# Kernel optimization log

Measured on AMD Instinct MI355X. Metric: run time of the kernel, lower is better.

Reference implementation:

```python
import jax, jax.numpy as jnp
import numpy as np

H, W, C = 64, 64, 128
HEADS, DIM_HEAD = 4, 32
DIM = HEADS * DIM_HEAD
SCALE = 10.0
EPS = 1e-08


def setup_inputs() -> dict:
    key = jax.random.key(0)
    k1, k2, k3, k4 = jax.random.split(key, 4)
    x = jax.random.normal(k1, (H, W, C), dtype=jnp.float32)
    # 1x1 conv kernels act as plain channel-mixing matrices
    w_in = jax.random.normal(k2, (3 * DIM, C), dtype=jnp.float32) * (1.0 / np.sqrt(C))
    w_out = jax.random.normal(k3, (C, DIM), dtype=jnp.float32) * (1.0 / np.sqrt(DIM))
    b_out = jax.random.normal(k4, (C,), dtype=jnp.float32) * 0.01
    return {"x": x, "w_in": w_in, "w_out": w_out, "b_out": b_out}


def reference(x, w_in, w_out, b_out):
    HW = H * W
    # conv_in: 1x1 conv == channel matmul -> (HW, 3, heads, dim_head)
    qkv = jnp.einsum('hwc,oc->hwo', x, w_in).reshape(HW, 3, HEADS, DIM_HEAD)
    q, k, v = qkv[:, 0], qkv[:, 1], qkv[:, 2]  # each (HW, h, d)

    def normalize(t):
        # L2 norm over the sequence axis (axis=0), as in the source
        n = jnp.sqrt(jnp.sum(t * t, axis=0, keepdims=True))
        return t / jnp.clip(n, EPS)

    q = normalize(q)
    k = normalize(k)
    sim = jnp.einsum('ihd,jhd->hij', q, k) * SCALE  # (h, HW, HW)
    attn = jax.nn.softmax(sim, axis=-1)
    out = jnp.einsum('hij,jhd->hid', attn, v)  # (h, HW, d)
    # 'h (H W) d -> H W (h d)'
    out = out.transpose(1, 0, 2).reshape(H, W, DIM)
    # conv_out: 1x1 conv with bias
    out = jnp.einsum('hwd,cd->hwc', out, w_out) + b_out
    return out
```

## Files before the change

kernel.cpp:

```cpp
#include <hip/hip_runtime.h>
#include <hip/hip_bf16.h>


typedef float  f32x4 __attribute__((ext_vector_type(4)));
typedef short  s16x8 __attribute__((ext_vector_type(8)));
typedef unsigned short u16x4 __attribute__((ext_vector_type(4)));
typedef unsigned short u16;

__device__ __forceinline__ u16 f2bf(float f) {
  unsigned int u = __float_as_uint(f);
  u += 0x7FFFu + ((u >> 16) & 1u);
  return (u16)(u >> 16);
}
__device__ __forceinline__ float bf2f(u16 u) {
  return __uint_as_float(((unsigned int)u) << 16);
}
__device__ __forceinline__ s16x8 load8f_bf16(const float* p) {
  const f32x4* q = (const f32x4*)p;
  f32x4 a = q[0], b = q[1];
  s16x8 r;
  r[0]=(short)f2bf(a[0]); r[1]=(short)f2bf(a[1]); r[2]=(short)f2bf(a[2]); r[3]=(short)f2bf(a[3]);
  r[4]=(short)f2bf(b[0]); r[5]=(short)f2bf(b[1]); r[6]=(short)f2bf(b[2]); r[7]=(short)f2bf(b[3]);
  return r;
}

__global__ __launch_bounds__(256) void qkv_kernel(
    const float* __restrict__ x, const float* __restrict__ w_in,
    u16* __restrict__ Qb, u16* __restrict__ Kb, u16* __restrict__ Vtb,
    float* __restrict__ part_sq) {
  __shared__ float sqpart[2][128];
  const int tid = threadIdx.x;
  const int w = tid >> 6, lane = tid & 63, li = lane & 15, kg = lane >> 4;
  const int wm = w & 1, wn = w >> 1;
  const int g = blockIdx.y;
  const int mb = blockIdx.x;
  const int irow = mb * 32 + wm * 16;

  s16x8 ax[4];
#pragma unroll
  for (int kc = 0; kc < 4; ++kc)
    ax[kc] = load8f_bf16(x + (size_t)(irow + li) * 128 + kc * 32 + kg * 8);

  const float* W = w_in + (size_t)g * 128 * 128;
#pragma unroll
  for (int nt = 0; nt < 4; ++nt) {
    const int colrel = wn * 64 + nt * 16 + li;
    f32x4 acc = {0.f, 0.f, 0.f, 0.f};
#pragma unroll
    for (int kc = 0; kc < 4; ++kc) {
      s16x8 bw = load8f_bf16(W + (size_t)colrel * 128 + kc * 32 + kg * 8);
      acc = __builtin_amdgcn_mfma_f32_16x16x32_bf16(ax[kc], bw, acc, 0, 0, 0);
    }
    const int h = colrel >> 5, d = colrel & 31;
    const int r0 = irow + kg * 4;
    if (g == 2) {
      u16x4 pv;
#pragma unroll
      for (int r = 0; r < 4; ++r) pv[r] = f2bf(acc[r]);
      *(u16x4*)(Vtb + ((size_t)(h * 32 + d) * 4096 + r0)) = pv;
    } else {
      float ss = acc[0]*acc[0] + acc[1]*acc[1] + acc[2]*acc[2] + acc[3]*acc[3];
      ss += __shfl_xor(ss, 16);
      ss += __shfl_xor(ss, 32);
      if (lane < 16) sqpart[wm][colrel] = ss;
      u16* dst = (g == 0 ? Qb : Kb);
#pragma unroll
      for (int r = 0; r < 4; ++r)
        dst[((size_t)h * 4096 + r0 + r) * 32 + d] = f2bf(acc[r]);
    }
  }
  __syncthreads();
  if (g < 2 && tid < 128)
    part_sq[((size_t)g * 128 + tid) * 128 + mb] = sqpart[0][tid] + sqpart[1][tid];
}

__global__ __launch_bounds__(1024, 4) void attn_kernel(
    const u16* __restrict__ Qb, const u16* __restrict__ Kb,
    const u16* __restrict__ Vtb, const float* __restrict__ part_sq,
    float* __restrict__ Oat, float* __restrict__ denom) {
  __shared__ __align__(16) char lds[99456];
  const int tid = threadIdx.x;
  const int w = tid >> 6, lane = tid & 63, li = lane & 15, kg = lane >> 4;
  const int wq = w >> 2, wk = w & 3;
  const int h = blockIdx.y, q0 = blockIdx.x * 64;
  float* dl  = (float*)(lds + 98304);
  float* scs = (float*)(lds + 99328);
  const u16* Kh = Kb  + (size_t)h * 4096 * 32;
  const u16* Vh = Vtb + (size_t)h * 32 * 4096;
  const int jl = tid >> 2, sl = tid & 3;
  const int dv = tid >> 5, sv = tid & 31;

  {
    s16x8 kreg = *(const s16x8*)(Kh + (size_t)jl * 32 + sl * 8);
    s16x8 vreg = *(const s16x8*)(Vh + (size_t)dv * 4096 + sv * 8);
    *(s16x8*)(lds + jl * 64 + ((sl * 16) ^ ((jl & 7) << 4))) = kreg;
    *(s16x8*)(lds + 32768 + dv * 512 + ((sv * 16) ^ ((dv & 7) << 4))) = vreg;
  }
  if (w == 0) {
    const int kind = lane >> 5, d = lane & 31;
    const f32x4* p4 = (const f32x4*)(part_sq + (size_t)(kind * 128 + h * 32 + d) * 128);
    float sum = 0.f;
#pragma unroll
    for (int m = 0; m < 32; ++m) { f32x4 v = p4[m]; sum += (v[0]+v[1]) + (v[2]+v[3]); }
    float n = fmaxf(sqrtf(sum), 1e-8f);
    float other = __shfl_xor(n, 32);
    if (lane < 32) scs[lane] = 10.f / (n * other);
  }
  __syncthreads();

  s16x8 aq;
  {
    const u16* qp = Qb + ((size_t)h * 4096 + q0 + wq * 16 + li) * 32 + kg * 8;
    s16x8 qr = *(const s16x8*)qp;
#pragma unroll
    for (int e = 0; e < 8; ++e) aq[e] = (short)f2bf(bf2f((u16)qr[e]) * scs[kg * 8 + e]);
  }

  f32x4 acc0 = {0,0,0,0}, acc1 = {0,0,0,0};
  float sden = 0.f;
  const int psw  = (li & 7) << 4;
  char* Pslab = lds + 65536 + w * 2048 + li * 128;
  const int kswz = (kg * 16) ^ psw;

  int cur = 0;
  for (int jt = 0; jt < 16; ++jt) {
    s16x8 kreg = {}, vreg = {};
    if (jt < 15) {
      const int j0n = (jt + 1) * 256;
      kreg = *(const s16x8*)(Kh + (size_t)(j0n + jl) * 32 + sl * 8);
      vreg = *(const s16x8*)(Vh + (size_t)dv * 4096 + j0n + sv * 8);
    }
    const char* Kc = lds + cur * 16384;
    const char* Vc = lds + 32768 + cur * 16384;
    f32x4 st[4];
#pragma unroll
    for (int jb = 0; jb < 4; ++jb) {
      s16x8 kf = *(const s16x8*)(Kc + (wk * 64 + jb * 16 + li) * 64 + kswz);
      f32x4 z = {0, 0, 0, 0};
      st[jb] = __builtin_amdgcn_mfma_f32_16x16x32_bf16(kf, aq, z, 0, 0, 0);
    }
#pragma unroll
    for (int jb = 0; jb < 4; ++jb) {
      float p0 = __expf(st[jb][0]), p1 = __expf(st[jb][1]);
      float p2 = __expf(st[jb][2]), p3 = __expf(st[jb][3]);
      sden += (p0 + p1) + (p2 + p3);
      uint2 pk;
      pk.x = (unsigned)f2bf(p0) | ((unsigned)f2bf(p1) << 16);
      pk.y = (unsigned)f2bf(p2) | ((unsigned)f2bf(p3) << 16);
      *(uint2*)(Pslab + ((jb * 32 + kg * 8) ^ psw)) = pk;
    }
#pragma unroll
    for (int c = 0; c < 2; ++c) {
      s16x8 ap = *(const s16x8*)(Pslab + ((c * 64 + kg * 16) ^ psw));
      const int vsw = ((wk * 8 + c * 4 + kg) * 16) ^ psw;
      s16x8 vf0 = *(const s16x8*)(Vc + li * 512 + vsw);
      s16x8 vf1 = *(const s16x8*)(Vc + (li + 16) * 512 + vsw);
      acc0 = __builtin_amdgcn_mfma_f32_16x16x32_bf16(ap, vf0, acc0, 0, 0, 0);
      acc1 = __builtin_amdgcn_mfma_f32_16x16x32_bf16(ap, vf1, acc1, 0, 0, 0);
    }
    __syncthreads();
    if (jt < 15) {
      char* Kn = lds + (cur ^ 1) * 16384;
      char* Vn = lds + 32768 + (cur ^ 1) * 16384;
      *(s16x8*)(Kn + jl * 64 + ((sl * 16) ^ ((jl & 7) << 4))) = kreg;
      *(s16x8*)(Vn + dv * 512 + ((sv * 16) ^ ((dv & 7) << 4))) = vreg;
    }
    __syncthreads();
    cur ^= 1;
  }

  sden += __shfl_xor(sden, 16);
  sden += __shfl_xor(sden, 32);
  if (lane < 16) dl[w * 16 + li] = sden;
  float* comb = (float*)lds;
#pragma unroll
  for (int r = 0; r < 4; ++r) {
    comb[(w * 16 + kg * 4 + r) * 32 + li]      = acc0[r];
    comb[(w * 16 + kg * 4 + r) * 32 + 16 + li] = acc1[r];
  }
  __syncthreads();
  {
    const int row = tid >> 4, cp = (tid & 15) * 2;
    const int wb = (row >> 4) * 4, r16 = row & 15;
    float o0 = 0.f, o1 = 0.f;
#pragma unroll
    for (int k2 = 0; k2 < 4; ++k2) {
      const float* src = comb + ((wb + k2) * 16 + r16) * 32 + cp;
      o0 += src[0]; o1 += src[1];
    }
    float2 o2 = {o0, o1};
    *(float2*)(Oat + (size_t)(q0 + row) * 128 + h * 32 + cp) = o2;
    if (tid < 64) {
      float ds = 0.f;
#pragma unroll
      for (int k2 = 0; k2 < 4; ++k2) ds += dl[((tid >> 4) * 4 + k2) * 16 + (tid & 15)];
      denom[(size_t)h * 4096 + q0 + tid] = ds;
    }
  }
}

__global__ __launch_bounds__(256) void proj_kernel(
    const float* __restrict__ Oat, const float* __restrict__ denom,
    const float* __restrict__ w_out, const float* __restrict__ b_out,
    float* __restrict__ out) {
  const int tid = threadIdx.x;
  const int w = tid >> 6, lane = tid & 63, li = lane & 15, kg = lane >> 4;
  const int i0 = blockIdx.x * 16;
  const int n0 = blockIdx.y * 64;
  const int i = i0 + li;

  s16x8 ao[4];
#pragma unroll
  for (int kc = 0; kc < 4; ++kc) {
    const float inv = 1.f / denom[(size_t)kc * 4096 + i];
    const f32x4* p = (const f32x4*)(Oat + (size_t)i * 128 + kc * 32 + kg * 8);
    f32x4 a = p[0], b = p[1];
    s16x8 r;
    r[0]=(short)f2bf(a[0]*inv); r[1]=(short)f2bf(a[1]*inv);
    r[2]=(short)f2bf(a[2]*inv); r[3]=(short)f2bf(a[3]*inv);
    r[4]=(short)f2bf(b[0]*inv); r[5]=(short)f2bf(b[1]*inv);
    r[6]=(short)f2bf(b[2]*inv); r[7]=(short)f2bf(b[3]*inv);
    ao[kc] = r;
  }
  const int c = n0 + w * 16 + li;
  f32x4 acc = {0, 0, 0, 0};
#pragma unroll
  for (int kc = 0; kc < 4; ++kc) {
    s16x8 bw = load8f_bf16(w_out + (size_t)c * 128 + kc * 32 + kg * 8);
    acc = __builtin_amdgcn_mfma_f32_16x16x32_bf16(ao[kc], bw, acc, 0, 0, 0);
  }
  const float bias = b_out[c];
#pragma unroll
  for (int r = 0; r < 4; ++r)
    out[(size_t)(i0 + kg * 4 + r) * 128 + c] = acc[r] + bias;
}

extern "C" void kernel_launch(void* const* d_in, const int* in_sizes, int n_in,
                              void* d_out, int out_size, void* d_ws, size_t ws_size,
                              hipStream_t stream) {
  const float* x     = (const float*)d_in[0];
  const float* w_in  = (const float*)d_in[1];
  const float* w_out = (const float*)d_in[2];
  const float* b_out = (const float*)d_in[3];
  float* out = (float*)d_out;

  char* ws = (char*)d_ws;
  float* Oat     = (float*)ws;
  float* denom   = (float*)(ws + 2097152);
  float* part_sq = (float*)(ws + 2097152 + 65536);
  u16*   Qb  = (u16*)(ws + 2097152 + 65536 + 131072);
  u16*   Kb  = (u16*)(ws + 2097152 + 65536 + 131072 + 1048576);
  u16*   Vtb = (u16*)(ws + 2097152 + 65536 + 131072 + 2 * 1048576);

  qkv_kernel <<<dim3(128, 3), 256,  0, stream>>>(x, w_in, Qb, Kb, Vtb, part_sq);
  attn_kernel<<<dim3(64, 4),  1024, 0, stream>>>(Qb, Kb, Vtb, part_sq, Oat, denom);
  proj_kernel<<<dim3(256, 2), 256,  0, stream>>>(Oat, denom, w_out, b_out, out);
}
```

Before: 102.2 us.

## Fuse QKV, attention and projection into one cooperative kernel with grid syncs

```diff
diff --git a/kernel.cpp b/kernel.cpp
--- a/kernel.cpp
+++ b/kernel.cpp
@@ -1,5 +1,7 @@
 #include <hip/hip_runtime.h>
 #include <hip/hip_bf16.h>
+#include <hip/hip_cooperative_groups.h>
+namespace cg = cooperative_groups;
 
 
 typedef float  f32x4 __attribute__((ext_vector_type(4)));
@@ -24,215 +26,199 @@
   return r;
 }
 
-__global__ __launch_bounds__(256) void qkv_kernel(
+__global__ __launch_bounds__(1024, 4) void fused_kernel(
     const float* __restrict__ x, const float* __restrict__ w_in,
+    const float* __restrict__ w_out, const float* __restrict__ b_out,
     u16* __restrict__ Qb, u16* __restrict__ Kb, u16* __restrict__ Vtb,
-    float* __restrict__ part_sq) {
-  __shared__ float sqpart[2][128];
-  const int tid = threadIdx.x;
-  const int w = tid >> 6, lane = tid & 63, li = lane & 15, kg = lane >> 4;
-  const int wm = w & 1, wn = w >> 1;
-  const int g = blockIdx.y;
-  const int mb = blockIdx.x;
-  const int irow = mb * 32 + wm * 16;
-
-  s16x8 ax[4];
-#pragma unroll
-  for (int kc = 0; kc < 4; ++kc)
-    ax[kc] = load8f_bf16(x + (size_t)(irow + li) * 128 + kc * 32 + kg * 8);
-
-  const float* W = w_in + (size_t)g * 128 * 128;
-#pragma unroll
-  for (int nt = 0; nt < 4; ++nt) {
-    const int colrel = wn * 64 + nt * 16 + li;
-    f32x4 acc = {0.f, 0.f, 0.f, 0.f};
-#pragma unroll
-    for (int kc = 0; kc < 4; ++kc) {
-      s16x8 bw = load8f_bf16(W + (size_t)colrel * 128 + kc * 32 + kg * 8);
-      acc = __builtin_amdgcn_mfma_f32_16x16x32_bf16(ax[kc], bw, acc, 0, 0, 0);
-    }
-    const int h = colrel >> 5, d = colrel & 31;
-    const int r0 = irow + kg * 4;
-    if (g == 2) {
-      u16x4 pv;
-#pragma unroll
-      for (int r = 0; r < 4; ++r) pv[r] = f2bf(acc[r]);
-      *(u16x4*)(Vtb + ((size_t)(h * 32 + d) * 4096 + r0)) = pv;
-    } else {
-      float ss = acc[0]*acc[0] + acc[1]*acc[1] + acc[2]*acc[2] + acc[3]*acc[3];
-      ss += __shfl_xor(ss, 16);
-      ss += __shfl_xor(ss, 32);
-      if (lane < 16) sqpart[wm][colrel] = ss;
-      u16* dst = (g == 0 ? Qb : Kb);
-#pragma unroll
-      for (int r = 0; r < 4; ++r)
-        dst[((size_t)h * 4096 + r0 + r) * 32 + d] = f2bf(acc[r]);
-    }
-  }
-  __syncthreads();
-  if (g < 2 && tid < 128)
-    part_sq[((size_t)g * 128 + tid) * 128 + mb] = sqpart[0][tid] + sqpart[1][tid];
-}
-
-__global__ __launch_bounds__(1024, 4) void attn_kernel(
-    const u16* __restrict__ Qb, const u16* __restrict__ Kb,
-    const u16* __restrict__ Vtb, const float* __restrict__ part_sq,
-    float* __restrict__ Oat, float* __restrict__ denom) {
+    float* __restrict__ sq, float* __restrict__ Oat,
+    float* __restrict__ denom, float* __restrict__ out) {
   __shared__ __align__(16) char lds[99456];
   const int tid = threadIdx.x;
   const int w = tid >> 6, lane = tid & 63, li = lane & 15, kg = lane >> 4;
-  const int wq = w >> 2, wk = w & 3;
-  const int h = blockIdx.y, q0 = blockIdx.x * 64;
-  float* dl  = (float*)(lds + 98304);
-  float* scs = (float*)(lds + 99328);
-  const u16* Kh = Kb  + (size_t)h * 4096 * 32;
-  const u16* Vh = Vtb + (size_t)h * 32 * 4096;
-  const int jl = tid >> 2, sl = tid & 3;
-  const int dv = tid >> 5, sv = tid & 31;
+  const int b = blockIdx.x;
 
   {
-    s16x8 kreg = *(const s16x8*)(Kh + (size_t)jl * 32 + sl * 8);
-    s16x8 vreg = *(const s16x8*)(Vh + (size_t)dv * 4096 + sv * 8);
-    *(s16x8*)(lds + jl * 64 + ((sl * 16) ^ ((jl & 7) << 4))) = kreg;
-    *(s16x8*)(lds + 32768 + dv * 512 + ((sv * 16) ^ ((dv & 7) << 4))) = vreg;
+    const int r0 = b * 16;
+    s16x8 ax[4];
+#pragma unroll
+    for (int kc = 0; kc < 4; ++kc)
+      ax[kc] = load8f_bf16(x + (size_t)(r0 + li) * 128 + kc * 32 + kg * 8);
+    for (int t = w; t < 24; t += 16) {
+      const int c = t * 16 + li;
+      f32x4 acc = {0.f, 0.f, 0.f, 0.f};
+#pragma unroll
+      for (int kc = 0; kc < 4; ++kc) {
+        s16x8 bw = load8f_bf16(w_in + (size_t)c * 128 + kc * 32 + kg * 8);
+        acc = __builtin_amdgcn_mfma_f32_16x16x32_bf16(ax[kc], bw, acc, 0, 0, 0);
+      }
+      const int g = c >> 7, colrel = c & 127;
+      const int h2 = colrel >> 5, d = colrel & 31;
+      const int rr = r0 + kg * 4;
+      if (g == 2) {
+        u16x4 pv;
+#pragma unroll
+        for (int r = 0; r < 4; ++r) pv[r] = f2bf(acc[r]);
+        *(u16x4*)(Vtb + ((size_t)(h2 * 32 + d) * 4096 + rr)) = pv;
+      } else {
+        float ss = acc[0]*acc[0] + acc[1]*acc[1] + acc[2]*acc[2] + acc[3]*acc[3];
+        ss += __shfl_xor(ss, 16);
+        ss += __shfl_xor(ss, 32);
+        u16* dst = (g == 0 ? Qb : Kb);
+#pragma unroll
+        for (int r = 0; r < 4; ++r)
+          dst[((size_t)h2 * 4096 + rr + r) * 32 + d] = f2bf(acc[r]);
+        if (lane < 16) atomicAdd(sq + g * 128 + colrel, ss);
+      }
+    }
   }
-  if (w == 0) {
-    const int kind = lane >> 5, d = lane & 31;
-    const f32x4* p4 = (const f32x4*)(part_sq + (size_t)(kind * 128 + h * 32 + d) * 128);
-    float sum = 0.f;
-#pragma unroll
-    for (int m = 0; m < 32; ++m) { f32x4 v = p4[m]; sum += (v[0]+v[1]) + (v[2]+v[3]); }
-    float n = fmaxf(sqrtf(sum), 1e-8f);
-    float other = __shfl_xor(n, 32);
-    if (lane < 32) scs[lane] = 10.f / (n * other);
+  __threadfence();
+  cg::this_grid().sync();
+
+  {
+    const int h = b >> 6, q0 = (b & 63) * 64;
+    const int wq = w >> 2, wk = w & 3;
+    float* dl  = (float*)(lds + 98304);
+    float* scs = (float*)(lds + 99328);
+    const u16* Kh = Kb  + (size_t)h * 4096 * 32;
+    const u16* Vh = Vtb + (size_t)h * 32 * 4096;
+    const int jl = tid >> 2, sl = tid & 3;
+    const int dv = tid >> 5, sv = tid & 31;
+
+    {
+      s16x8 kreg = *(const s16x8*)(Kh + (size_t)jl * 32 + sl * 8);
+      s16x8 vreg = *(const s16x8*)(Vh + (size_t)dv * 4096 + sv * 8);
+      *(s16x8*)(lds + jl * 64 + ((sl * 16) ^ ((jl & 7) << 4))) = kreg;
+      *(s16x8*)(lds + 32768 + dv * 512 + ((sv * 16) ^ ((dv & 7) << 4))) = vreg;
+    }
+    if (w == 0) {
+      const int kind = lane >> 5, d = lane & 31;
+      float n = fmaxf(sqrtf(sq[kind * 128 + h * 32 + d]), 1e-8f);
+      float other = __shfl_xor(n, 32);
+      if (lane < 32) scs[lane] = 10.f / (n * other);
+    }
+    __syncthreads();
+
+    s16x8 aq;
+    {
+      const u16* qp = Qb + ((size_t)h * 4096 + q0 + wq * 16 + li) * 32 + kg * 8;
+      s16x8 qr = *(const s16x8*)qp;
+#pragma unroll
+      for (int e = 0; e < 8; ++e) aq[e] = (short)f2bf(bf2f((u16)qr[e]) * scs[kg * 8 + e]);
+    }
+
+    f32x4 acc0 = {0,0,0,0}, acc1 = {0,0,0,0};
+    float sden = 0.f;
+    const int psw  = (li & 7) << 4;
+    char* Pslab = lds + 65536 + w * 2048 + li * 128;
+    const int kswz = (kg * 16) ^ psw;
+
+    int cur = 0;
+    for (int jt = 0; jt < 16; ++jt) {
+      s16x8 kreg = {}, vreg = {};
+      if (jt < 15) {
+        const int j0n = (jt + 1) * 256;
+        kreg = *(const s16x8*)(Kh + (size_t)(j0n + jl) * 32 + sl * 8);
+        vreg = *(const s16x8*)(Vh + (size_t)dv * 4096 + j0n + sv * 8);
+      }
+      const char* Kc = lds + cur * 16384;
+      const char* Vc = lds + 32768 + cur * 16384;
+      f32x4 st[4];
+#pragma unroll
+      for (int jb = 0; jb < 4; ++jb) {
+        s16x8 kf = *(const s16x8*)(Kc + (wk * 64 + jb * 16 + li) * 64 + kswz);
+        f32x4 z = {0, 0, 0, 0};
+        st[jb] = __builtin_amdgcn_mfma_f32_16x16x32_bf16(kf, aq, z, 0, 0, 0);
+      }
+#pragma unroll
+      for (int jb = 0; jb < 4; ++jb) {
+        float p0 = __expf(st[jb][0]), p1 = __expf(st[jb][1]);
+        float p2 = __expf(st[jb][2]), p3 = __expf(st[jb][3]);
+        sden += (p0 + p1) + (p2 + p3);
+        uint2 pk;
+        pk.x = (unsigned)f2bf(p0) | ((unsigned)f2bf(p1) << 16);
+        pk.y = (unsigned)f2bf(p2) | ((unsigned)f2bf(p3) << 16);
+        *(uint2*)(Pslab + ((jb * 32 + kg * 8) ^ psw)) = pk;
+      }
+#pragma unroll
+      for (int c = 0; c < 2; ++c) {
+        s16x8 ap = *(const s16x8*)(Pslab + ((c * 64 + kg * 16) ^ psw));
+        const int vsw = ((wk * 8 + c * 4 + kg) * 16) ^ psw;
+        s16x8 vf0 = *(const s16x8*)(Vc + li * 512 + vsw);
+        s16x8 vf1 = *(const s16x8*)(Vc + (li + 16) * 512 + vsw);
+        acc0 = __builtin_amdgcn_mfma_f32_16x16x32_bf16(ap, vf0, acc0, 0, 0, 0);
+        acc1 = __builtin_amdgcn_mfma_f32_16x16x32_bf16(ap, vf1, acc1, 0, 0, 0);
+      }
+      __syncthreads();
+      if (jt < 15) {
+        char* Kn = lds + (cur ^ 1) * 16384;
+        char* Vn = lds + 32768 + (cur ^ 1) * 16384;
+        *(s16x8*)(Kn + jl * 64 + ((sl * 16) ^ ((jl & 7) << 4))) = kreg;
+        *(s16x8*)(Vn + dv * 512 + ((sv * 16) ^ ((dv & 7) << 4))) = vreg;
+      }
+      __syncthreads();
+      cur ^= 1;
+    }
+
+    sden += __shfl_xor(sden, 16);
+    sden += __shfl_xor(sden, 32);
+    if (lane < 16) dl[w * 16 + li] = sden;
+    float* comb = (float*)lds;
+#pragma unroll
+    for (int r = 0; r < 4; ++r) {
+      comb[(w * 16 + kg * 4 + r) * 32 + li]      = acc0[r];
+      comb[(w * 16 + kg * 4 + r) * 32 + 16 + li] = acc1[r];
+    }
+    __syncthreads();
+    {
+      const int row = tid >> 4, cp = (tid & 15) * 2;
+      const int wb = (row >> 4) * 4, r16 = row & 15;
+      float o0 = 0.f, o1 = 0.f;
+#pragma unroll
+      for (int k2 = 0; k2 < 4; ++k2) {
+        const float* src = comb + ((wb + k2) * 16 + r16) * 32 + cp;
+        o0 += src[0]; o1 += src[1];
+      }
+      float2 o2 = {o0, o1};
+      *(float2*)(Oat + (size_t)(q0 + row) * 128 + h * 32 + cp) = o2;
+      if (tid < 64) {
+        float ds = 0.f;
+#pragma unroll
+        for (int k2 = 0; k2 < 4; ++k2) ds += dl[((tid >> 4) * 4 + k2) * 16 + (tid & 15)];
+        denom[(size_t)h * 4096 + q0 + tid] = ds;
+      }
+    }
   }
-  __syncthreads();
-
-  s16x8 aq;
-  {
-    const u16* qp = Qb + ((size_t)h * 4096 + q0 + wq * 16 + li) * 32 + kg * 8;
-    s16x8 qr = *(const s16x8*)qp;
-#pragma unroll
-    for (int e = 0; e < 8; ++e) aq[e] = (short)f2bf(bf2f((u16)qr[e]) * scs[kg * 8 + e]);
+  __threadfence();
+  cg::this_grid().sync();
+
+  if (w < 8) {
+    const int i0 = b * 16;
+    const int i = i0 + li;
+    s16x8 ao[4];
+#pragma unroll
+    for (int kc = 0; kc < 4; ++kc) {
+      const float inv = 1.f / denom[(size_t)kc * 4096 + i];
+      const f32x4* p = (const f32x4*)(Oat + (size_t)i * 128 + kc * 32 + kg * 8);
+      f32x4 a = p[0], bb = p[1];
+      s16x8 r;
+      r[0]=(short)f2bf(a[0]*inv);  r[1]=(short)f2bf(a[1]*inv);
+      r[2]=(short)f2bf(a[2]*inv);  r[3]=(short)f2bf(a[3]*inv);
+      r[4]=(short)f2bf(bb[0]*inv); r[5]=(short)f2bf(bb[1]*inv);
+      r[6]=(short)f2bf(bb[2]*inv); r[7]=(short)f2bf(bb[3]*inv);
+      ao[kc] = r;
+    }
+    const int c = w * 16 + li;
+    f32x4 acc = {0, 0, 0, 0};
+#pragma unroll
+    for (int kc = 0; kc < 4; ++kc) {
+      s16x8 bw = load8f_bf16(w_out + (size_t)c * 128 + kc * 32 + kg * 8);
+      acc = __builtin_amdgcn_mfma_f32_16x16x32_bf16(ao[kc], bw, acc, 0, 0, 0);
+    }
+    const float bias = b_out[c];
+#pragma unroll
+    for (int r = 0; r < 4; ++r)
+      out[(size_t)(i0 + kg * 4 + r) * 128 + c] = acc[r] + bias;
   }
-
-  f32x4 acc0 = {0,0,0,0}, acc1 = {0,0,0,0};
-  float sden = 0.f;
-  const int psw  = (li & 7) << 4;
-  char* Pslab = lds + 65536 + w * 2048 + li * 128;
-  const int kswz = (kg * 16) ^ psw;
-
-  int cur = 0;
-  for (int jt = 0; jt < 16; ++jt) {
-    s16x8 kreg = {}, vreg = {};
-    if (jt < 15) {
-      const int j0n = (jt + 1) * 256;
-      kreg = *(const s16x8*)(Kh + (size_t)(j0n + jl) * 32 + sl * 8);
-      vreg = *(const s16x8*)(Vh + (size_t)dv * 4096 + j0n + sv * 8);
-    }
-    const char* Kc = lds + cur * 16384;
-    const char* Vc = lds + 32768 + cur * 16384;
-    f32x4 st[4];
-#pragma unroll
-    for (int jb = 0; jb < 4; ++jb) {
-      s16x8 kf = *(const s16x8*)(Kc + (wk * 64 + jb * 16 + li) * 64 + kswz);
-      f32x4 z = {0, 0, 0, 0};
-      st[jb] = __builtin_amdgcn_mfma_f32_16x16x32_bf16(kf, aq, z, 0, 0, 0);
-    }
-#pragma unroll
-    for (int jb = 0; jb < 4; ++jb) {
-      float p0 = __expf(st[jb][0]), p1 = __expf(st[jb][1]);
-      float p2 = __expf(st[jb][2]), p3 = __expf(st[jb][3]);
-      sden += (p0 + p1) + (p2 + p3);
-      uint2 pk;
-      pk.x = (unsigned)f2bf(p0) | ((unsigned)f2bf(p1) << 16);
-      pk.y = (unsigned)f2bf(p2) | ((unsigned)f2bf(p3) << 16);
-      *(uint2*)(Pslab + ((jb * 32 + kg * 8) ^ psw)) = pk;
-    }
-#pragma unroll
-    for (int c = 0; c < 2; ++c) {
-      s16x8 ap = *(const s16x8*)(Pslab + ((c * 64 + kg * 16) ^ psw));
-      const int vsw = ((wk * 8 + c * 4 + kg) * 16) ^ psw;
-      s16x8 vf0 = *(const s16x8*)(Vc + li * 512 + vsw);
-      s16x8 vf1 = *(const s16x8*)(Vc + (li + 16) * 512 + vsw);
-      acc0 = __builtin_amdgcn_mfma_f32_16x16x32_bf16(ap, vf0, acc0, 0, 0, 0);
-      acc1 = __builtin_amdgcn_mfma_f32_16x16x32_bf16(ap, vf1, acc1, 0, 0, 0);
-    }
-    __syncthreads();
-    if (jt < 15) {
-      char* Kn = lds + (cur ^ 1) * 16384;
-      char* Vn = lds + 32768 + (cur ^ 1) * 16384;
-      *(s16x8*)(Kn + jl * 64 + ((sl * 16) ^ ((jl & 7) << 4))) = kreg;
-      *(s16x8*)(Vn + dv * 512 + ((sv * 16) ^ ((dv & 7) << 4))) = vreg;
-    }
-    __syncthreads();
-    cur ^= 1;
-  }
-
-  sden += __shfl_xor(sden, 16);
-  sden += __shfl_xor(sden, 32);
-  if (lane < 16) dl[w * 16 + li] = sden;
-  float* comb = (float*)lds;
-#pragma unroll
-  for (int r = 0; r < 4; ++r) {
-    comb[(w * 16 + kg * 4 + r) * 32 + li]      = acc0[r];
-    comb[(w * 16 + kg * 4 + r) * 32 + 16 + li] = acc1[r];
-  }
-  __syncthreads();
-  {
-    const int row = tid >> 4, cp = (tid & 15) * 2;
-    const int wb = (row >> 4) * 4, r16 = row & 15;
-    float o0 = 0.f, o1 = 0.f;
-#pragma unroll
-    for (int k2 = 0; k2 < 4; ++k2) {
-      const float* src = comb + ((wb + k2) * 16 + r16) * 32 + cp;
-      o0 += src[0]; o1 += src[1];
-    }
-    float2 o2 = {o0, o1};
-    *(float2*)(Oat + (size_t)(q0 + row) * 128 + h * 32 + cp) = o2;
-    if (tid < 64) {
-      float ds = 0.f;
-#pragma unroll
-      for (int k2 = 0; k2 < 4; ++k2) ds += dl[((tid >> 4) * 4 + k2) * 16 + (tid & 15)];
-      denom[(size_t)h * 4096 + q0 + tid] = ds;
-    }
-  }
-}
-
-__global__ __launch_bounds__(256) void proj_kernel(
-    const float* __restrict__ Oat, const float* __restrict__ denom,
-    const float* __restrict__ w_out, const float* __restrict__ b_out,
-    float* __restrict__ out) {
-  const int tid = threadIdx.x;
-  const int w = tid >> 6, lane = tid & 63, li = lane & 15, kg = lane >> 4;
-  const int i0 = blockIdx.x * 16;
-  const int n0 = blockIdx.y * 64;
-  const int i = i0 + li;
-
-  s16x8 ao[4];
-#pragma unroll
-  for (int kc = 0; kc < 4; ++kc) {
-    const float inv = 1.f / denom[(size_t)kc * 4096 + i];
-    const f32x4* p = (const f32x4*)(Oat + (size_t)i * 128 + kc * 32 + kg * 8);
-    f32x4 a = p[0], b = p[1];
-    s16x8 r;
-    r[0]=(short)f2bf(a[0]*inv); r[1]=(short)f2bf(a[1]*inv);
-    r[2]=(short)f2bf(a[2]*inv); r[3]=(short)f2bf(a[3]*inv);
-    r[4]=(short)f2bf(b[0]*inv); r[5]=(short)f2bf(b[1]*inv);
-    r[6]=(short)f2bf(b[2]*inv); r[7]=(short)f2bf(b[3]*inv);
-    ao[kc] = r;
-  }
-  const int c = n0 + w * 16 + li;
-  f32x4 acc = {0, 0, 0, 0};
-#pragma unroll
-  for (int kc = 0; kc < 4; ++kc) {
-    s16x8 bw = load8f_bf16(w_out + (size_t)c * 128 + kc * 32 + kg * 8);
-    acc = __builtin_amdgcn_mfma_f32_16x16x32_bf16(ao[kc], bw, acc, 0, 0, 0);
-  }
-  const float bias = b_out[c];
-#pragma unroll
-  for (int r = 0; r < 4; ++r)
-    out[(size_t)(i0 + kg * 4 + r) * 128 + c] = acc[r] + bias;
 }
 
 extern "C" void kernel_launch(void* const* d_in, const int* in_sizes, int n_in,
@@ -245,14 +231,17 @@
   float* out = (float*)d_out;
 
   char* ws = (char*)d_ws;
-  float* Oat     = (float*)ws;
-  float* denom   = (float*)(ws + 2097152);
-  float* part_sq = (float*)(ws + 2097152 + 65536);
-  u16*   Qb  = (u16*)(ws + 2097152 + 65536 + 131072);
-  u16*   Kb  = (u16*)(ws + 2097152 + 65536 + 131072 + 1048576);
-  u16*   Vtb = (u16*)(ws + 2097152 + 65536 + 131072 + 2 * 1048576);
-
-  qkv_kernel <<<dim3(128, 3), 256,  0, stream>>>(x, w_in, Qb, Kb, Vtb, part_sq);
-  attn_kernel<<<dim3(64, 4),  1024, 0, stream>>>(Qb, Kb, Vtb, part_sq, Oat, denom);
-  proj_kernel<<<dim3(256, 2), 256,  0, stream>>>(Oat, denom, w_out, b_out, out);
-}
+  float* Oat   = (float*)ws;
+  float* denom = (float*)(ws + 2097152);
+  float* sq    = (float*)(ws + 2097152 + 65536);
+  u16*   Qb  = (u16*)(ws + 2097152 + 65536 + 1024);
+  u16*   Kb  = (u16*)(ws + 2097152 + 65536 + 1024 + 1048576);
+  u16*   Vtb = (u16*)(ws + 2097152 + 65536 + 1024 + 2 * 1048576);
+
+  hipMemsetAsync(sq, 0, 1024, stream);
+  void* args[] = {(void*)&x, (void*)&w_in, (void*)&w_out, (void*)&b_out,
+                  (void*)&Qb, (void*)&Kb, (void*)&Vtb, (void*)&sq,
+                  (void*)&Oat, (void*)&denom, (void*)&out};
+  hipLaunchCooperativeKernel((const void*)fused_kernel, dim3(256), dim3(1024),
+                             args, 0, stream);
+}
```

Result: slower. 343.7 us (+236.2%).
